# Optimization experiments

Measured on AMD Instinct MI355X. Metric: run time of the kernel, lower is better.

Reference implementation:

```python
import jax, jax.numpy as jnp
import numpy as np

N_NODES = 100000      # total nodes across batch (50 graphs x 2000 nodes)
N_EDGES = 1600000     # avg degree 16
D = 64                # input_dim = hidden dims = output_dim
L = 3                 # number of GIN layers actually executed
NUM_GRAPHS = 50
NODES_PER_GRAPH = 2000
CAT_D = L * D         # 192, concat of hidden layer outputs


def setup_inputs() -> dict:
    key = jax.random.key(0)
    ks = jax.random.split(key, 12)
    s = 1.0 / np.sqrt(D)          # torch Linear init scale
    s2 = 1.0 / np.sqrt(CAT_D)
    return {
        "x": jax.random.normal(ks[0], (N_NODES, D), jnp.float32),
        "edge_index": jax.random.randint(ks[1], (2, N_EDGES), 0, N_NODES),
        "edge_weight": jax.random.uniform(ks[2], (N_EDGES,), jnp.float32),
        "batch": jnp.repeat(jnp.arange(NUM_GRAPHS), NODES_PER_GRAPH),  # sorted graph ids
        "W1": jax.random.uniform(ks[3], (L, D, D), jnp.float32, -s, s),
        "b1": jax.random.uniform(ks[4], (L, D), jnp.float32, -s, s),
        "W2": jax.random.uniform(ks[5], (L, D, D), jnp.float32, -s, s),
        "b2": jax.random.uniform(ks[6], (L, D), jnp.float32, -s, s),
        "eps": jnp.zeros((L,), jnp.float32),  # train_eps init 0.0
        "lin_w": jax.random.uniform(ks[7], (CAT_D, D), jnp.float32, -s2, s2),
        "lin_b": jax.random.uniform(ks[8], (D,), jnp.float32, -s2, s2),
    }


def reference(x, edge_index, edge_weight, batch, W1, b1, W2, b2, eps, lin_w, lin_b):
    src, dst = edge_index[0], edge_index[1]
    ew = edge_weight[:, None]
    h = x
    hiddens = []
    for l in range(L):
        # weighted GIN: aggregate sum_j w_ij * h_j at destination nodes
        agg = jax.ops.segment_sum(h[src] * ew, dst, num_segments=N_NODES)
        z = (1.0 + eps[l]) * h + agg
        # GIN MLP: Linear -> LeakyReLU -> Linear
        z = jax.nn.leaky_relu(z @ W1[l] + b1[l]) @ W2[l] + b2[l]
        hiddens.append(z)              # hiddens store pre-activation conv output
        h = jax.nn.leaky_relu(z)       # activation feeds next layer (dropout=0)
    h_cat = jnp.concatenate(hiddens, axis=-1)          # [N, 192]
    pooled = jax.ops.segment_sum(h_cat, batch, num_segments=NUM_GRAPHS)  # global_add_pool
    return pooled @ lin_w + lin_b                      # [NUM_GRAPHS, D]
```

## Files before the change

### kernel.cpp

```cpp
#include <hip/hip_runtime.h>

#define N_NODES 100000
#define N_EDGES 1600000
#define DD 64
#define NLAYER 3
#define NUM_GRAPHS 50
#define NODES_PER_GRAPH 2000
#define CAT_D (NLAYER * DD)
#define MROWS 80
#define MLP_THREADS 320
#define LPITCH 72

#define NPB 256
#define NB ((N_NODES + NPB - 1) / NPB)
#define BPAD 6144
#define ECHUNK 4096

#define GNODES 32
#define WECAP 384

typedef __attribute__((ext_vector_type(8))) short short8;
typedef __attribute__((ext_vector_type(4))) float float4v;
typedef __attribute__((ext_vector_type(2))) float float2v;

__device__ __forceinline__ unsigned short f2bf(float f) {
    unsigned u = __float_as_uint(f);
    unsigned r = u + 0x7FFF + ((u >> 16) & 1);
    return (unsigned short)(r >> 16);
}
__device__ __forceinline__ float bflo(unsigned u) {
    return __uint_as_float(u << 16);
}
__device__ __forceinline__ float bfhi(unsigned u) {
    return __uint_as_float(u & 0xFFFF0000u);
}

__global__ __launch_bounds__(256) void convert_x_kernel(
    const float* __restrict__ x, uint2* __restrict__ hx8)
{
    int i = blockIdx.x * blockDim.x + threadIdx.x;
    if (i < N_NODES * DD / 8) {
        const float4* xp = (const float4*)(x + (size_t)i * 8);
        float4 a = xp[0], b = xp[1];
        int lo = 0, hi = 0;
        lo = __builtin_amdgcn_cvt_pk_fp8_f32(a.x, a.y, lo, 0);
        lo = __builtin_amdgcn_cvt_pk_fp8_f32(a.z, a.w, lo, 1);
        hi = __builtin_amdgcn_cvt_pk_fp8_f32(b.x, b.y, hi, 0);
        hi = __builtin_amdgcn_cvt_pk_fp8_f32(b.z, b.w, hi, 1);
        uint2 o; o.x = (unsigned)lo; o.y = (unsigned)hi;
        hx8[i] = o;
    }
}

__global__ __launch_bounds__(256) void convert_w_kernel(
    const float* __restrict__ W1, const float* __restrict__ W2,
    unsigned short* __restrict__ W1t, unsigned short* __restrict__ W2t,
    int* __restrict__ cursor)
{
    int idx = blockIdx.x * blockDim.x + threadIdx.x;
    if (idx < NB) cursor[idx] = idx * BPAD;
    if (idx >= 2 * NLAYER * DD * DD) return;
    int which = idx / (NLAYER * DD * DD);
    int rem = idx % (NLAYER * DD * DD);
    int l = rem / (DD * DD);
    int t = rem % (DD * DD);
    int n = t >> 6, k = t & 63;
    const float* W = which ? W2 : W1;
    unsigned short* Wt = which ? W2t : W1t;
    Wt[l * DD * DD + n * DD + k] = f2bf(W[l * DD * DD + k * DD + n]);
}

__global__ __launch_bounds__(256) void bin_kernel(
    const int* __restrict__ src, const int* __restrict__ dst,
    const float* __restrict__ ew, int* __restrict__ cursor,
    uint2* __restrict__ binned)
{
    __shared__ uint2 stage[ECHUNK];
    __shared__ unsigned short bkt[ECHUNK];
    __shared__ int cnt[512];
    __shared__ int base[512];
    __shared__ int ssum[256];
    __shared__ int gbase[512];

    const int tid = threadIdx.x;
    const int start = blockIdx.x * ECHUNK;
    const int count = min(ECHUNK, N_EDGES - start);

    cnt[tid] = 0;
    cnt[tid + 256] = 0;
    __syncthreads();

    unsigned pk1[16], pk2[16];
    int eb[16], er[16];
    #pragma unroll
    for (int k = 0; k < 16; ++k) {
        int i = tid + k * 256;
        if (i < count) {
            int e = start + i;
            int s = src[e];
            int d = dst[e];
            float w = ew[e];
            int b = d >> 8;
            pk1[k] = (unsigned)s | ((unsigned)(d & 255) << 17);
            pk2[k] = __float_as_uint(w);
            eb[k] = b;
            er[k] = atomicAdd(&cnt[b], 1);
        } else {
            eb[k] = -1;
        }
    }
    __syncthreads();

    int c0 = cnt[2 * tid], c1 = cnt[2 * tid + 1];
    ssum[tid] = c0 + c1;
    __syncthreads();
    for (int off = 1; off < 256; off <<= 1) {
        int x = (tid >= off) ? ssum[tid - off] : 0;
        __syncthreads();
        ssum[tid] += x;
        __syncthreads();
    }
    int ex = (tid > 0) ? ssum[tid - 1] : 0;
    base[2 * tid] = ex;
    base[2 * tid + 1] = ex + c0;

    if (2 * tid < NB && c0 > 0)     gbase[2 * tid]     = atomicAdd(&cursor[2 * tid], c0);
    if (2 * tid + 1 < NB && c1 > 0) gbase[2 * tid + 1] = atomicAdd(&cursor[2 * tid + 1], c1);
    __syncthreads();

    #pragma unroll
    for (int k = 0; k < 16; ++k) {
        if (eb[k] >= 0) {
            int p = base[eb[k]] + er[k];
            stage[p].x = pk1[k];
            stage[p].y = pk2[k];
            bkt[p] = (unsigned short)eb[k];
        }
    }
    __syncthreads();

    for (int i = tid; i < count; i += 256) {
        int b = bkt[i];
        binned[gbase[b] + (i - base[b])] = stage[i];
    }
}

__global__ __launch_bounds__(256) void localsort_kernel(
    const int* __restrict__ cursor, const uint2* __restrict__ binned,
    unsigned* __restrict__ s_edge, int* __restrict__ beg, int* __restrict__ end)
{
    __shared__ int deg[NPB];
    __shared__ int rb[NPB];
    __shared__ int cur[NPB];

    const int nb = blockIdx.x;
    const int tid = threadIdx.x;
    const int bstart = nb * BPAD;
    const int count = cursor[nb] - bstart;

    deg[tid] = 0;
    __syncthreads();
    for (int i = tid; i < count; i += 256) {
        unsigned w = binned[bstart + i].x;
        atomicAdd(&deg[(w >> 17) & 255], 1);
    }
    __syncthreads();

    int v = deg[tid];
    rb[tid] = v;
    __syncthreads();
    for (int off = 1; off < 256; off <<= 1) {
        int x = (tid >= off) ? rb[tid - off] : 0;
        __syncthreads();
        rb[tid] += x;
        __syncthreads();
    }
    int ex = rb[tid] - v;
    cur[tid] = ex;
    int node = nb * NPB + tid;
    if (node < N_NODES) {
        beg[node] = bstart + ex;
        end[node] = bstart + ex + v;
    }
    __syncthreads();

    for (int i = tid; i < count; i += 256) {
        uint2 e = binned[bstart + i];
        int d = (e.x >> 17) & 255;
        int r = atomicAdd(&cur[d], 1);
        unsigned wb = (unsigned)f2bf(__uint_as_float(e.y)) & 0x7FFF;
        s_edge[bstart + r] = (e.x & 0x1FFFF) | (wb << 17);
    }
}

__global__ __launch_bounds__(256) void gather_kernel(
    const uint2* __restrict__ h8, const int* __restrict__ beg,
    const int* __restrict__ end, const unsigned* __restrict__ s_edge,
    const float* __restrict__ eps, int l, uint4* __restrict__ z4)
{
    __shared__ unsigned eds[4 * WECAP];

    const int w    = threadIdx.x >> 6;
    const int lane = threadIdx.x & 63;
    const int o    = lane >> 3;
    const int fl   = lane & 7;
    const int nbase = blockIdx.x * GNODES + w * 8;
    const int node  = nbase + o;

    const int ebeg = beg[nbase];
    const int cnt  = end[nbase + 7] - ebeg;
    unsigned* wl = &eds[w * WECAP];
    const bool lds_ok = (cnt <= WECAP);
    if (lds_ok) {
        for (int i = lane; i < cnt; i += 64) wl[i] = s_edge[ebeg + i];
    }

    const int gbeg = beg[node];
    const int deg  = end[node] - gbeg;

    float acc[4][8];
    #pragma unroll
    for (int c = 0; c < 4; ++c)
        #pragma unroll
        for (int j = 0; j < 8; ++j) acc[c][j] = 0.f;

    const uint2* hfl = h8 + fl;

    if (lds_ok) {
        const int bi = gbeg - ebeg;
        for (int it = 0; it < deg; it += 4) {
            #pragma unroll
            for (int c = 0; c < 4; ++c) {
                bool ok = (it + c) < deg;
                int idx = ok ? (bi + it + c) : bi;
                unsigned p = wl[idx];
                float wv = ok ? __uint_as_float((p >> 17) << 16) : 0.f;
                uint2 r = hfl[(long)(p & 0x1FFFF) * 8];
                float2v f01 = __builtin_amdgcn_cvt_pk_f32_fp8(r.x, false);
                float2v f23 = __builtin_amdgcn_cvt_pk_f32_fp8(r.x, true);
                float2v f45 = __builtin_amdgcn_cvt_pk_f32_fp8(r.y, false);
                float2v f67 = __builtin_amdgcn_cvt_pk_f32_fp8(r.y, true);
                acc[c][0] += f01.x * wv;  acc[c][1] += f01.y * wv;
                acc[c][2] += f23.x * wv;  acc[c][3] += f23.y * wv;
                acc[c][4] += f45.x * wv;  acc[c][5] += f45.y * wv;
                acc[c][6] += f67.x * wv;  acc[c][7] += f67.y * wv;
            }
        }
    } else {
        for (int it = 0; it < deg; it += 4) {
            #pragma unroll
            for (int c = 0; c < 4; ++c) {
                bool ok = (it + c) < deg;
                int idx = ok ? (gbeg + it + c) : gbeg;
                unsigned p = s_edge[idx];
                float wv = ok ? __uint_as_float((p >> 17) << 16) : 0.f;
                uint2 r = hfl[(long)(p & 0x1FFFF) * 8];
                float2v f01 = __builtin_amdgcn_cvt_pk_f32_fp8(r.x, false);
                float2v f23 = __builtin_amdgcn_cvt_pk_f32_fp8(r.x, true);
                float2v f45 = __builtin_amdgcn_cvt_pk_f32_fp8(r.y, false);
                float2v f67 = __builtin_amdgcn_cvt_pk_f32_fp8(r.y, true);
                acc[c][0] += f01.x * wv;  acc[c][1] += f01.y * wv;
                acc[c][2] += f23.x * wv;  acc[c][3] += f23.y * wv;
                acc[c][4] += f45.x * wv;  acc[c][5] += f45.y * wv;
                acc[c][6] += f67.x * wv;  acc[c][7] += f67.y * wv;
            }
        }
    }

    float s[8];
    #pragma unroll
    for (int j = 0; j < 8; ++j)
        s[j] = (acc[0][j] + acc[1][j]) + (acc[2][j] + acc[3][j]);

    const float e1 = 1.0f + eps[l];
    uint2 selfr = hfl[(long)node * 8];
    float2v s01 = __builtin_amdgcn_cvt_pk_f32_fp8(selfr.x, false);
    float2v s23 = __builtin_amdgcn_cvt_pk_f32_fp8(selfr.x, true);
    float2v s45 = __builtin_amdgcn_cvt_pk_f32_fp8(selfr.y, false);
    float2v s67 = __builtin_amdgcn_cvt_pk_f32_fp8(selfr.y, true);
    float z0 = e1 * s01.x + s[0];
    float z1 = e1 * s01.y + s[1];
    float z2 = e1 * s23.x + s[2];
    float z3 = e1 * s23.y + s[3];
    float z4v = e1 * s45.x + s[4];
    float z5 = e1 * s45.y + s[5];
    float z6 = e1 * s67.x + s[6];
    float z7 = e1 * s67.y + s[7];
    uint4 ov;
    ov.x = (unsigned)f2bf(z0) | ((unsigned)f2bf(z1) << 16);
    ov.y = (unsigned)f2bf(z2) | ((unsigned)f2bf(z3) << 16);
    ov.z = (unsigned)f2bf(z4v) | ((unsigned)f2bf(z5) << 16);
    ov.w = (unsigned)f2bf(z6) | ((unsigned)f2bf(z7) << 16);
    z4[(long)node * 8 + fl] = ov;
}

__global__ __launch_bounds__(MLP_THREADS) void mlp_kernel(
    const unsigned short* __restrict__ z_in,
    const unsigned short* __restrict__ W1t, const unsigned short* __restrict__ W2t,
    const float* __restrict__ b1l, const float* __restrict__ b2l,
    int l, uint2* __restrict__ h_out8, float* __restrict__ pooled)
{
    __shared__ __align__(16) unsigned short zs[MROWS * LPITCH];
    __shared__ __align__(16) unsigned short w1s[DD * LPITCH];
    __shared__ __align__(16) unsigned short w2s[DD * LPITCH];
    __shared__ float red[5 * DD];

    const int tid  = threadIdx.x;
    const int lane = tid & 63;
    const int w    = tid >> 6;
    const int m15  = lane & 15;
    const int quad = lane >> 4;
    const long base = (long)blockIdx.x * MROWS;

    for (int idx = tid; idx < MROWS * 8; idx += MLP_THREADS) {
        int row = idx >> 3, seg = idx & 7;
        *(int4*)&zs[row * LPITCH + seg * 8] =
            *(const int4*)&z_in[(base + row) * DD + seg * 8];
    }
    for (int idx = tid; idx < DD * 8; idx += MLP_THREADS) {
        int row = idx >> 3, seg = idx & 7;
        *(int4*)&w1s[row * LPITCH + seg * 8] =
            *(const int4*)&W1t[(size_t)l * DD * DD + row * DD + seg * 8];
        *(int4*)&w2s[row * LPITCH + seg * 8] =
            *(const int4*)&W2t[(size_t)l * DD * DD + row * DD + seg * 8];
    }
    __syncthreads();

    {
        short8 a0 = *(const short8*)&zs[(w * 16 + m15) * LPITCH + quad * 8];
        short8 a1 = *(const short8*)&zs[(w * 16 + m15) * LPITCH + 32 + quad * 8];
        #pragma unroll
        for (int n = 0; n < 4; ++n) {
            short8 b0 = *(const short8*)&w1s[(n * 16 + m15) * LPITCH + quad * 8];
            short8 b1 = *(const short8*)&w1s[(n * 16 + m15) * LPITCH + 32 + quad * 8];
            float4v acc = {0.f, 0.f, 0.f, 0.f};
            acc = __builtin_amdgcn_mfma_f32_16x16x32_bf16(a0, b0, acc, 0, 0, 0);
            acc = __builtin_amdgcn_mfma_f32_16x16x32_bf16(a1, b1, acc, 0, 0, 0);
            int col = n * 16 + m15;
            float bv = b1l[col];
            #pragma unroll
            for (int r = 0; r < 4; ++r) {
                int row = w * 16 + quad * 4 + r;
                float t = acc[r] + bv;
                t = t > 0.0f ? t : 0.01f * t;
                zs[row * LPITCH + col] = f2bf(t);
            }
        }
    }

    float psum[4];
    {
        short8 a0 = *(const short8*)&zs[(w * 16 + m15) * LPITCH + quad * 8];
        short8 a1 = *(const short8*)&zs[(w * 16 + m15) * LPITCH + 32 + quad * 8];
        #pragma unroll
        for (int n = 0; n < 4; ++n) {
            short8 b0 = *(const short8*)&w2s[(n * 16 + m15) * LPITCH + quad * 8];
            short8 b1 = *(const short8*)&w2s[(n * 16 + m15) * LPITCH + 32 + quad * 8];
            float4v acc = {0.f, 0.f, 0.f, 0.f};
            acc = __builtin_amdgcn_mfma_f32_16x16x32_bf16(a0, b0, acc, 0, 0, 0);
            acc = __builtin_amdgcn_mfma_f32_16x16x32_bf16(a1, b1, acc, 0, 0, 0);
            int col = n * 16 + m15;
            float bv = b2l[col];
            float ps = 0.0f;
            #pragma unroll
            for (int r = 0; r < 4; ++r) {
                int row = w * 16 + quad * 4 + r;
                float z2 = acc[r] + bv;
                ps += z2;
                float hv = z2 > 0.0f ? z2 : 0.01f * z2;
                zs[row * LPITCH + col] = f2bf(hv);
            }
            psum[n] = ps;
        }
    }
    #pragma unroll
    for (int n = 0; n < 4; ++n) {
        float v = psum[n];
        v += __shfl_xor(v, 16);
        v += __shfl_xor(v, 32);
        if (quad == 0) red[w * DD + n * 16 + m15] = v;
    }
    __syncthreads();

    if (h_out8) {
        for (int idx = tid; idx < MROWS * 8; idx += MLP_THREADS) {
            int row = idx >> 3, seg = idx & 7;
            int4 v = *(const int4*)&zs[row * LPITCH + seg * 8];
            int lo = 0, hi = 0;
            lo = __builtin_amdgcn_cvt_pk_fp8_f32(bflo((unsigned)v.x), bfhi((unsigned)v.x), lo, 0);
            lo = __builtin_amdgcn_cvt_pk_fp8_f32(bflo((unsigned)v.y), bfhi((unsigned)v.y), lo, 1);
            hi = __builtin_amdgcn_cvt_pk_fp8_f32(bflo((unsigned)v.z), bfhi((unsigned)v.z), hi, 0);
            hi = __builtin_amdgcn_cvt_pk_fp8_f32(bflo((unsigned)v.w), bfhi((unsigned)v.w), hi, 1);
            uint2 o; o.x = (unsigned)lo; o.y = (unsigned)hi;
            h_out8[(base + row) * 8 + seg] = o;
        }
    }
    if (tid < DD) {
        float tot = red[tid] + red[DD + tid] + red[2 * DD + tid]
                  + red[3 * DD + tid] + red[4 * DD + tid];
        int g = blockIdx.x / (NODES_PER_GRAPH / MROWS);
        atomicAdd(&pooled[g * CAT_D + l * DD + tid], tot);
    }
}

__global__ __launch_bounds__(64) void final_kernel(
    const float* __restrict__ pooled, const float* __restrict__ lin_w,
    const float* __restrict__ lin_b, float* __restrict__ out)
{
    int g = blockIdx.x;
    int j = threadIdx.x;
    float acc = lin_b[j];
    for (int k = 0; k < CAT_D; ++k)
        acc += pooled[g * CAT_D + k] * lin_w[k * DD + j];
    out[g * DD + j] = acc;
}

extern "C" void kernel_launch(void* const* d_in, const int* in_sizes, int n_in,
                              void* d_out, int out_size, void* d_ws, size_t ws_size,
                              hipStream_t stream)
{
    const float* x     = (const float*)d_in[0];
    const int*   ei    = (const int*)d_in[1];
    const float* ew    = (const float*)d_in[2];
    const float* W1    = (const float*)d_in[4];
    const float* b1    = (const float*)d_in[5];
    const float* W2    = (const float*)d_in[6];
    const float* b2    = (const float*)d_in[7];
    const float* eps   = (const float*)d_in[8];
    const float* lin_w = (const float*)d_in[9];
    const float* lin_b = (const float*)d_in[10];
    float* out = (float*)d_out;

    const int* src = ei;
    const int* dst = ei + N_EDGES;

    char* wsb = (char*)d_ws;
    size_t off = 0;
    auto alloc = [&](size_t bytes) -> void* {
        off = (off + 15) & ~(size_t)15;
        void* p = wsb + off;
        off += bytes;
        return p;
    };
    uint2*  hX    = (uint2*)alloc((size_t)N_NODES * DD);
    uint2*  hA    = (uint2*)alloc((size_t)N_NODES * DD);
    unsigned short* zbuf = (unsigned short*)alloc((size_t)N_NODES * DD * 2);
    unsigned short* W1t  = (unsigned short*)alloc((size_t)NLAYER * DD * DD * 2);
    unsigned short* W2t  = (unsigned short*)alloc((size_t)NLAYER * DD * DD * 2);
    float* pooled        = (float*)alloc((size_t)NUM_GRAPHS * CAT_D * 4);
    int*   cursor        = (int*)alloc((size_t)NB * 4);
    int*   beg           = (int*)alloc((size_t)N_NODES * 4);
    int*   end_          = (int*)alloc((size_t)N_NODES * 4);
    uint2* binned        = (uint2*)alloc((size_t)NB * BPAD * 8);
    unsigned* s_edge     = (unsigned*)alloc((size_t)NB * BPAD * 4);

    convert_x_kernel<<<(N_NODES * DD / 8 + 255) / 256, 256, 0, stream>>>(x, hX);
    convert_w_kernel<<<(2 * NLAYER * DD * DD + 255) / 256, 256, 0, stream>>>(
        W1, W2, W1t, W2t, cursor);

    bin_kernel<<<(N_EDGES + ECHUNK - 1) / ECHUNK, 256, 0, stream>>>(
        src, dst, ew, cursor, binned);
    localsort_kernel<<<NB, 256, 0, stream>>>(cursor, binned, s_edge, beg, end_);

    hipMemsetAsync(pooled, 0, NUM_GRAPHS * CAT_D * sizeof(float), stream);

    const uint2* h_ins[3]  = { hX, hA, hX };
    uint2*       h_outs[3] = { hA, hX, nullptr };
    for (int l = 0; l < NLAYER; ++l) {
        gather_kernel<<<N_NODES / GNODES, 256, 0, stream>>>(
            h_ins[l], beg, end_, s_edge, eps, l, (uint4*)zbuf);

        mlp_kernel<<<N_NODES / MROWS, MLP_THREADS, 0, stream>>>(
            zbuf, W1t, W2t,
            b1 + (size_t)l * DD, b2 + (size_t)l * DD,
            l, h_outs[l], pooled);
    }

    final_kernel<<<NUM_GRAPHS, 64, 0, stream>>>(pooled, lin_w, lin_b, out);
}
```

Measured before the change: 244.8 us.

## Pack edge records early into split arrays and fold weight conversion into binning

The binning kernel now packs source and bf16 weight into one 32-bit record and writes the local destination as a separate byte array, instead of writing 8-byte records. Localsort then reads only the byte array for degree counting and copies the packed word without converting it again. This cuts intermediate traffic from 8 to 5 bytes per edge. The weight-transpose kernel is merged into extra blocks of the bin kernel and the cursor init moves into convert_x, which removes one launch.

```diff
diff --git a/kernel.cpp b/kernel.cpp
--- a/kernel.cpp
+++ b/kernel.cpp
@@ -15,6 +15,8 @@
 #define NB ((N_NODES + NPB - 1) / NPB)
 #define BPAD 6144
 #define ECHUNK 4096
+#define NBBIN ((N_EDGES + ECHUNK - 1) / ECHUNK)
+#define NWCONV ((2 * NLAYER * DD * DD + 255) / 256)
 
 #define GNODES 32
 #define WECAP 384
@@ -36,9 +38,10 @@
 }
 
 __global__ __launch_bounds__(256) void convert_x_kernel(
-    const float* __restrict__ x, uint2* __restrict__ hx8)
+    const float* __restrict__ x, uint2* __restrict__ hx8, int* __restrict__ cursor)
 {
     int i = blockIdx.x * blockDim.x + threadIdx.x;
+    if (i < NB) cursor[i] = i * BPAD;
     if (i < N_NODES * DD / 8) {
         const float4* xp = (const float4*)(x + (size_t)i * 8);
         float4 a = xp[0], b = xp[1];
@@ -52,30 +55,29 @@
     }
 }
 
-__global__ __launch_bounds__(256) void convert_w_kernel(
-    const float* __restrict__ W1, const float* __restrict__ W2,
-    unsigned short* __restrict__ W1t, unsigned short* __restrict__ W2t,
-    int* __restrict__ cursor)
-{
-    int idx = blockIdx.x * blockDim.x + threadIdx.x;
-    if (idx < NB) cursor[idx] = idx * BPAD;
-    if (idx >= 2 * NLAYER * DD * DD) return;
-    int which = idx / (NLAYER * DD * DD);
-    int rem = idx % (NLAYER * DD * DD);
-    int l = rem / (DD * DD);
-    int t = rem % (DD * DD);
-    int n = t >> 6, k = t & 63;
-    const float* W = which ? W2 : W1;
-    unsigned short* Wt = which ? W2t : W1t;
-    Wt[l * DD * DD + n * DD + k] = f2bf(W[l * DD * DD + k * DD + n]);
-}
-
 __global__ __launch_bounds__(256) void bin_kernel(
     const int* __restrict__ src, const int* __restrict__ dst,
     const float* __restrict__ ew, int* __restrict__ cursor,
-    uint2* __restrict__ binned)
-{
-    __shared__ uint2 stage[ECHUNK];
+    unsigned* __restrict__ brec, unsigned char* __restrict__ bdloc,
+    const float* __restrict__ W1, const float* __restrict__ W2,
+    unsigned short* __restrict__ W1t, unsigned short* __restrict__ W2t)
+{
+    if (blockIdx.x >= NBBIN) {
+        int idx = (blockIdx.x - NBBIN) * 256 + threadIdx.x;
+        if (idx >= 2 * NLAYER * DD * DD) return;
+        int which = idx / (NLAYER * DD * DD);
+        int rem = idx % (NLAYER * DD * DD);
+        int l = rem / (DD * DD);
+        int t = rem % (DD * DD);
+        int n = t >> 6, k = t & 63;
+        const float* W = which ? W2 : W1;
+        unsigned short* Wt = which ? W2t : W1t;
+        Wt[l * DD * DD + n * DD + k] = f2bf(W[l * DD * DD + k * DD + n]);
+        return;
+    }
+
+    __shared__ unsigned stage[ECHUNK];
+    __shared__ unsigned char dstage[ECHUNK];
     __shared__ unsigned short bkt[ECHUNK];
     __shared__ int cnt[512];
     __shared__ int base[512];
@@ -90,7 +92,8 @@
     cnt[tid + 256] = 0;
     __syncthreads();
 
-    unsigned pk1[16], pk2[16];
+    unsigned pk[16];
+    unsigned char dl[16];
     int eb[16], er[16];
     #pragma unroll
     for (int k = 0; k < 16; ++k) {
@@ -101,8 +104,8 @@
             int d = dst[e];
             float w = ew[e];
             int b = d >> 8;
-            pk1[k] = (unsigned)s | ((unsigned)(d & 255) << 17);
-            pk2[k] = __float_as_uint(w);
+            pk[k] = (unsigned)s | (((unsigned)f2bf(w) & 0x7FFF) << 17);
+            dl[k] = (unsigned char)(d & 255);
             eb[k] = b;
             er[k] = atomicAdd(&cnt[b], 1);
         } else {
@@ -132,8 +135,8 @@
     for (int k = 0; k < 16; ++k) {
         if (eb[k] >= 0) {
             int p = base[eb[k]] + er[k];
-            stage[p].x = pk1[k];
-            stage[p].y = pk2[k];
+            stage[p] = pk[k];
+            dstage[p] = dl[k];
             bkt[p] = (unsigned short)eb[k];
         }
     }
@@ -141,12 +144,15 @@
 
     for (int i = tid; i < count; i += 256) {
         int b = bkt[i];
-        binned[gbase[b] + (i - base[b])] = stage[i];
+        int g = gbase[b] + (i - base[b]);
+        brec[g] = stage[i];
+        bdloc[g] = dstage[i];
     }
 }
 
 __global__ __launch_bounds__(256) void localsort_kernel(
-    const int* __restrict__ cursor, const uint2* __restrict__ binned,
+    const int* __restrict__ cursor, const unsigned* __restrict__ brec,
+    const unsigned char* __restrict__ bdloc,
     unsigned* __restrict__ s_edge, int* __restrict__ beg, int* __restrict__ end)
 {
     __shared__ int deg[NPB];
@@ -161,8 +167,7 @@
     deg[tid] = 0;
     __syncthreads();
     for (int i = tid; i < count; i += 256) {
-        unsigned w = binned[bstart + i].x;
-        atomicAdd(&deg[(w >> 17) & 255], 1);
+        atomicAdd(&deg[bdloc[bstart + i]], 1);
     }
     __syncthreads();
 
@@ -185,11 +190,9 @@
     __syncthreads();
 
     for (int i = tid; i < count; i += 256) {
-        uint2 e = binned[bstart + i];
-        int d = (e.x >> 17) & 255;
+        int d = bdloc[bstart + i];
         int r = atomicAdd(&cur[d], 1);
-        unsigned wb = (unsigned)f2bf(__uint_as_float(e.y)) & 0x7FFF;
-        s_edge[bstart + r] = (e.x & 0x1FFFF) | (wb << 17);
+        s_edge[bstart + r] = brec[bstart + i];
     }
 }
 
@@ -451,16 +454,15 @@
     int*   cursor        = (int*)alloc((size_t)NB * 4);
     int*   beg           = (int*)alloc((size_t)N_NODES * 4);
     int*   end_          = (int*)alloc((size_t)N_NODES * 4);
-    uint2* binned        = (uint2*)alloc((size_t)NB * BPAD * 8);
+    unsigned* brec       = (unsigned*)alloc((size_t)NB * BPAD * 4);
+    unsigned char* bdloc = (unsigned char*)alloc((size_t)NB * BPAD);
     unsigned* s_edge     = (unsigned*)alloc((size_t)NB * BPAD * 4);
 
-    convert_x_kernel<<<(N_NODES * DD / 8 + 255) / 256, 256, 0, stream>>>(x, hX);
-    convert_w_kernel<<<(2 * NLAYER * DD * DD + 255) / 256, 256, 0, stream>>>(
-        W1, W2, W1t, W2t, cursor);
-
-    bin_kernel<<<(N_EDGES + ECHUNK - 1) / ECHUNK, 256, 0, stream>>>(
-        src, dst, ew, cursor, binned);
-    localsort_kernel<<<NB, 256, 0, stream>>>(cursor, binned, s_edge, beg, end_);
+    convert_x_kernel<<<(N_NODES * DD / 8 + 255) / 256, 256, 0, stream>>>(x, hX, cursor);
+
+    bin_kernel<<<NBBIN + NWCONV, 256, 0, stream>>>(
+        src, dst, ew, cursor, brec, bdloc, W1, W2, W1t, W2t);
+    localsort_kernel<<<NB, 256, 0, stream>>>(cursor, brec, bdloc, s_edge, beg, end_);
 
     hipMemsetAsync(pooled, 0, NUM_GRAPHS * CAT_D * sizeof(float), stream);
 
```

Result: no change. 248.0 us (+1.3%).
